# Optimization experiments

Measured on AMD Instinct MI355X. Metric: run time of the kernel, lower is better.

The kernel has to match this reference:

```python
import jax, jax.numpy as jnp
import numpy as np

NUM_HEADS = 12
ROPE_THETA = 10000.0


def _rope_cos_sin(n, hd, dtype):
    inv_freq = 1.0 / (ROPE_THETA ** (np.arange(0, hd, 2, dtype=np.float64) / hd))
    freqs = np.outer(np.arange(n, dtype=np.float64), inv_freq)  # (N, hd/2)
    emb = np.concatenate([freqs, freqs], axis=-1)               # (N, hd)
    return jnp.asarray(np.cos(emb), dtype), jnp.asarray(np.sin(emb), dtype)


def _apply_rope(t, cos, sin):
    # t: (B, H, N, hd); rotate-half convention
    half = t.shape[-1] // 2
    t1, t2 = t[..., :half], t[..., half:]
    rot = jnp.concatenate([-t2, t1], axis=-1)
    return t * cos + rot * sin


def setup_inputs() -> dict:
    key = jax.random.key(0)
    k1, k2, k3 = jax.random.split(key, 3)
    B, N, C = 8, 1024, 768
    x = jax.random.normal(k1, (B, N, C), dtype=jnp.float32)
    w_qkv = jax.random.normal(k2, (C, 3 * C), dtype=jnp.float32) * 0.02
    w_proj = jax.random.normal(k3, (C, C), dtype=jnp.float32) * 0.02
    b_proj = jnp.zeros((C,), dtype=jnp.float32)
    return {"x": x, "w_qkv": w_qkv, "w_proj": w_proj, "b_proj": b_proj}


def reference(x, w_qkv, w_proj, b_proj):
    B, N, C = x.shape
    H = NUM_HEADS
    hd = C // H
    scale = hd ** -0.5
    # qkv: (B,N,3C) -> (B,N,3,H,hd) -> (B,H,3,N,hd)
    qkv = (x @ w_qkv).reshape(B, N, 3, H, hd).transpose(0, 3, 2, 1, 4)
    q, k, v = qkv[:, :, 0], qkv[:, :, 1], qkv[:, :, 2]  # each (B,H,N,hd)
    cos, sin = _rope_cos_sin(N, hd, x.dtype)
    q = _apply_rope(q, cos, sin)
    k = _apply_rope(k, cos, sin)
    attn = jax.nn.softmax(jnp.einsum("bhqd,bhkd->bhqk", q, k) * scale, axis=-1)
    out = jnp.einsum("bhqk,bhkd->bhqd", attn, v)  # (B,H,N,hd)
    out = out.transpose(0, 2, 1, 3).reshape(B, N, C)
    return out @ w_proj + b_proj
```

## Files before the change

### kernel.cpp

```cpp
#include <hip/hip_runtime.h>

typedef unsigned short ushort_t;
typedef __bf16 bf16x8 __attribute__((ext_vector_type(8)));
typedef float f32x4 __attribute__((ext_vector_type(4)));
typedef float f32x16 __attribute__((ext_vector_type(16)));
typedef unsigned short u16x8 __attribute__((ext_vector_type(8)));
typedef unsigned int u32x2 __attribute__((ext_vector_type(2)));
typedef unsigned int u32x4 __attribute__((ext_vector_type(4)));

#define MFMA16(a, b, c) __builtin_amdgcn_mfma_f32_16x16x32_bf16((a), (b), (c), 0, 0, 0)
#define MFMA32(a, b, c) __builtin_amdgcn_mfma_f32_32x32x16_bf16((a), (b), (c), 0, 0, 0)

#define SEQ 1024
#define NHEAD 12
#define HD 64
#define CDIM 768
#define TS 6291456
#define QSCALE 0.1803368801111204f

__device__ __forceinline__ ushort_t f2bf(float f) {
  __bf16 b = (__bf16)f;
  return __builtin_bit_cast(ushort_t, b);
}
__device__ __forceinline__ unsigned pk2(float lo, float hi) {
  return (unsigned)f2bf(lo) | ((unsigned)f2bf(hi) << 16);
}

__device__ __forceinline__ void plswap(unsigned &a, unsigned &b) {
  u32x2 r = __builtin_amdgcn_permlane32_swap(a, b, false, false);
  a = r[0];
  b = r[1];
}

typedef __attribute__((address_space(1))) void gvoid_t;
typedef __attribute__((address_space(3))) void lvoid_t;
__device__ __forceinline__ void async16(const ushort_t* g, ushort_t* l) {
  __builtin_amdgcn_global_load_lds((gvoid_t*)g, (lvoid_t*)l, 16, 0, 0);
}

__device__ __forceinline__ void transpose_body(const float* __restrict__ in,
                                               ushort_t* __restrict__ out,
                                               int R, int C, int bxi, int byi,
                                               float (*tile)[33]) {
  int bx = bxi * 32, by = byi * 32;
  int tx = threadIdx.x & 31, ty = threadIdx.x >> 5;
#pragma unroll
  for (int i = ty; i < 32; i += 8) {
    int r = by + i, c = bx + tx;
    if (r < R && c < C) tile[i][tx] = in[(size_t)r * C + c];
  }
  __syncthreads();
#pragma unroll
  for (int i = ty; i < 32; i += 8) {
    int r = bx + i, c = by + tx;
    if (r < C && c < R) out[(size_t)r * R + c] = f2bf(tile[tx][i]);
  }
}

__global__ void __launch_bounds__(256) prep_all(const float* __restrict__ x,
                                                const float* __restrict__ w_qkv,
                                                const float* __restrict__ w_proj,
                                                ushort_t* __restrict__ xb,
                                                ushort_t* __restrict__ wqkvT,
                                                ushort_t* __restrict__ wprojT,
                                                float* __restrict__ tab) {
  __shared__ float tile[32][33];
  const int bid = blockIdx.x;
  if (bid < 3072) {
    int i = (bid * 256 + threadIdx.x) * 8;
    float4 a = *(const float4*)(x + i);
    float4 b = *(const float4*)(x + i + 4);
    u16x8 r;
    r[0] = f2bf(a.x); r[1] = f2bf(a.y); r[2] = f2bf(a.z); r[3] = f2bf(a.w);
    r[4] = f2bf(b.x); r[5] = f2bf(b.y); r[6] = f2bf(b.z); r[7] = f2bf(b.w);
    *(u16x8*)(xb + i) = r;
  } else if (bid < 3072 + 1728) {
    int t = bid - 3072;
    transpose_body(w_qkv, wqkvT, 768, 2304, t % 72, t / 72, tile);
  } else if (bid < 3072 + 1728 + 576) {
    int t = bid - (3072 + 1728);
    transpose_body(w_proj, wprojT, 768, 768, t % 24, t / 24, tile);
  } else {
    int g = (bid - 5376) * 256 + threadIdx.x;
    int n = g >> 5, j = g & 31;
    double invf = pow(10000.0, -((double)(2 * j)) / 64.0);
    double fr = (double)n * invf;
    tab[g * 2]     = (float)cos(fr);
    tab[g * 2 + 1] = (float)sin(fr);
  }
}

__device__ __forceinline__ void gemm_compute32(const ushort_t* la, const ushort_t* lb,
                                               int wm, int wn, int fr, int fq,
                                               f32x4 acc[4][4]) {
  bf16x8 aF[4], bF[4];
#pragma unroll
  for (int i = 0; i < 4; ++i) {
    const int R = wm + i * 16 + fr;
    aF[i] = *(const bf16x8*)(la + R * 32 + (((fq + (R >> 1)) & 3) << 3));
  }
#pragma unroll
  for (int j = 0; j < 4; ++j) {
    const int S = wn + j * 16 + fr;
    bF[j] = *(const bf16x8*)(lb + S * 32 + (((fq + (S >> 1)) & 3) << 3));
  }
#pragma unroll
  for (int i = 0; i < 4; ++i)
#pragma unroll
    for (int j = 0; j < 4; ++j) acc[i][j] = MFMA16(aF[i], bF[j], acc[i][j]);
}

__device__ __forceinline__ void gemm_bt_core(const ushort_t* __restrict__ A,
                                             const ushort_t* __restrict__ Bt,
                                             int bm, int bn,
                                             ushort_t (*ldsA)[4096],
                                             ushort_t (*ldsB)[4096],
                                             f32x4 acc[4][4]) {
  const int tid = threadIdx.x;
  const int lane = tid & 63, wid = tid >> 6;
  const int wm = (wid >> 1) * 64, wn = (wid & 1) * 64;
  const int fr = lane & 15, fq = lane >> 4;
#pragma unroll
  for (int i = 0; i < 4; ++i)
#pragma unroll
    for (int j = 0; j < 4; ++j) acc[i][j] = (f32x4){0.f, 0.f, 0.f, 0.f};

  const int srow = tid >> 2;
  const int scol = (((tid & 3) - (srow >> 1)) & 3) << 3;
  const ushort_t* aSrc = A + (size_t)(bm + srow) * CDIM + scol;
  const ushort_t* bSrc = Bt + (size_t)(bn + srow) * CDIM + scol;

#define STAGE_STEP(buf, s)                                                       \
  {                                                                              \
    async16(aSrc + (s) * 32, ldsA[buf] + tid * 8);                               \
    async16(aSrc + (size_t)64 * CDIM + (s) * 32, ldsA[buf] + 2048 + tid * 8);    \
    async16(bSrc + (s) * 32, ldsB[buf] + tid * 8);                               \
    async16(bSrc + (size_t)64 * CDIM + (s) * 32, ldsB[buf] + 2048 + tid * 8);    \
  }

  STAGE_STEP(0, 0);
  STAGE_STEP(1, 1);
  STAGE_STEP(2, 2);

#pragma unroll 3
  for (int s = 0; s < 21; ++s) {
    const int b = s % 3;
    asm volatile("s_waitcnt vmcnt(8)" ::: "memory");
    __builtin_amdgcn_sched_barrier(0);
    __builtin_amdgcn_s_barrier();
    __builtin_amdgcn_sched_barrier(0);
    gemm_compute32(ldsA[b], ldsB[b], wm, wn, fr, fq, acc);
    __builtin_amdgcn_sched_barrier(0);
    __builtin_amdgcn_s_barrier();
    __builtin_amdgcn_sched_barrier(0);
    STAGE_STEP(b, s + 3);
  }
  asm volatile("s_waitcnt vmcnt(8)" ::: "memory");
  __builtin_amdgcn_sched_barrier(0);
  __builtin_amdgcn_s_barrier();
  __builtin_amdgcn_sched_barrier(0);
  gemm_compute32(ldsA[0], ldsB[0], wm, wn, fr, fq, acc);
  asm volatile("s_waitcnt vmcnt(4)" ::: "memory");
  __builtin_amdgcn_sched_barrier(0);
  __builtin_amdgcn_s_barrier();
  __builtin_amdgcn_sched_barrier(0);
  gemm_compute32(ldsA[1], ldsB[1], wm, wn, fr, fq, acc);
  asm volatile("s_waitcnt vmcnt(0)" ::: "memory");
  __builtin_amdgcn_sched_barrier(0);
  __builtin_amdgcn_s_barrier();
  __builtin_amdgcn_sched_barrier(0);
  gemm_compute32(ldsA[2], ldsB[2], wm, wn, fr, fq, acc);
#undef STAGE_STEP
}

__global__ void __launch_bounds__(256) gemm_qkv(const ushort_t* __restrict__ A,
                                                const ushort_t* __restrict__ Bt,
                                                const float* __restrict__ tab,
                                                ushort_t* __restrict__ qkv) {
  __shared__ __attribute__((aligned(16))) ushort_t ldsA[3][4096];
  __shared__ __attribute__((aligned(16))) ushort_t ldsB[3][4096];
  f32x4 acc[4][4];
  const int f = blockIdx.x;
  const int xcd = f & 7, r = f >> 3;
  const int bm = (xcd * 8 + (r & 7)) * 128;
  const int bn = (r >> 3) * 128;
  gemm_bt_core(A, Bt, bm, bn, ldsA, ldsB, acc);
  const int lane = threadIdx.x & 63, wid = threadIdx.x >> 6;
  const int wm = (wid >> 1) * 64, wn = (wid & 1) * 64;
  const int fr = lane & 15, fq = lane >> 4;
  const int tensor = bn / 768;

  if (tensor < 2) {
    ushort_t* dstT = qkv + (size_t)tensor * TS;
    const float qs = (tensor == 0) ? QSCALE : 1.0f;
#pragma unroll
    for (int i = 0; i < 4; ++i) {
#pragma unroll
      for (int jp = 0; jp < 2; ++jp) {
        const int col = bn + wn + jp * 16 + fr;
        const int rem = col - tensor * 768;
        const int h = rem >> 6;
        const int d2 = rem & 31;
#pragma unroll
        for (int rr = 0; rr < 4; ++rr) {
          const int row = bm + wm + i * 16 + fq * 4 + rr;
          const int b = row >> 10, n = row & 1023;
          const float2 cs = ((const float2*)tab)[n * 32 + d2];
          const float av = acc[i][jp][rr], bv = acc[i][jp + 2][rr];
          const float o1 = (av * cs.x - bv * cs.y) * qs;
          const float o2 = (bv * cs.x + av * cs.y) * qs;
          ushort_t* dst = dstT + ((size_t)(b * NHEAD + h) * SEQ + n) * HD + d2;
          dst[0]  = f2bf(o1);
          dst[32] = f2bf(o2);
        }
      }
    }
  } else {
    ushort_t* vt = qkv + 2 * (size_t)TS;
#pragma unroll
    for (int i = 0; i < 4; ++i) {
      const int row0 = bm + wm + i * 16 + fq * 4;
      const int b = row0 >> 10, n0 = row0 & 1023;
#pragma unroll
      for (int j = 0; j < 4; ++j) {
        const int col = bn + wn + j * 16 + fr;
        const int rem = col - 1536;
        const int h = rem >> 6, d = rem & 63;
        u32x2 pk;
        pk[0] = pk2(acc[i][j][0], acc[i][j][1]);
        pk[1] = pk2(acc[i][j][2], acc[i][j][3]);
        *(u32x2*)(vt + ((size_t)(b * NHEAD + h) * HD + d) * SEQ + n0) = pk;
      }
    }
  }
}

__global__ void __launch_bounds__(256) gemm_proj(const ushort_t* __restrict__ A,
                                                 const ushort_t* __restrict__ Bt,
                                                 const float* __restrict__ bias,
                                                 float* __restrict__ Cout) {
  __shared__ __attribute__((aligned(16))) ushort_t ldsA[3][4096];
  __shared__ __attribute__((aligned(16))) ushort_t ldsB[3][4096];
  f32x4 acc[4][4];
  const int f = blockIdx.x;
  const int xcd = f & 7, r = f >> 3;
  const int bm = (xcd * 8 + (r & 7)) * 128;
  const int bn = (r >> 3) * 128;
  gemm_bt_core(A, Bt, bm, bn, ldsA, ldsB, acc);
  const int lane = threadIdx.x & 63, wid = threadIdx.x >> 6;
  const int wm = (wid >> 1) * 64, wn = (wid & 1) * 64;
  const int fr = lane & 15, fq = lane >> 4;
#pragma unroll
  for (int i = 0; i < 4; ++i) {
#pragma unroll
    for (int j = 0; j < 4; ++j) {
      const int col = bn + wn + j * 16 + fr;
      const float bv = bias[col];
#pragma unroll
      for (int rr = 0; rr < 4; ++rr) {
        const int row = bm + wm + i * 16 + fq * 4 + rr;
        Cout[(size_t)row * CDIM + col] = acc[i][j][rr] + bv;
      }
    }
  }
}

__global__ void __launch_bounds__(256) attn_fused(const ushort_t* __restrict__ Qb,
                                                  const ushort_t* __restrict__ Kb,
                                                  const ushort_t* __restrict__ VTb,
                                                  ushort_t* __restrict__ Ob) {
  __shared__ __attribute__((aligned(16))) ushort_t ldsK[2][4096];
  __shared__ __attribute__((aligned(16))) ushort_t ldsV[2][4096];

  const int tid = threadIdx.x, lane = tid & 63, wid = tid >> 6;
  const int l31 = lane & 31, h = lane >> 5;

  const int f = blockIdx.x;
  const int xp = f & 7, rest = f >> 3;
  const int g = rest % 12, qb = rest / 12;
  const int head = g * 8 + xp;
  const int q0 = qb * 128;

  const ushort_t* Qh  = Qb  + (size_t)head * (SEQ * HD);
  const ushort_t* Kh  = Kb  + (size_t)head * (SEQ * HD);
  const ushort_t* VTh = VTb + (size_t)head * (HD * SEQ);

  const int qrow = q0 + wid * 32 + l31;
  bf16x8 qF[4];
#pragma unroll
  for (int dk = 0; dk < 4; ++dk)
    qF[dk] = *(const bf16x8*)(Qh + (size_t)qrow * HD + dk * 16 + 8 * h);

  f32x16 ot[2];
#pragma unroll
  for (int dt = 0; dt < 2; ++dt)
#pragma unroll
    for (int i = 0; i < 16; ++i) ot[dt][i] = 0.f;
  float lsum = 0.f;

  const int s0 = tid, s1 = tid + 256;
  const int r0 = s0 >> 3, c0 = ((s0 & 7) - r0) & 7;
  const int r1 = s1 >> 3, c1 = ((s1 & 7) - r1) & 7;

#define ASTAGE(buf, kt)                                                         \
  {                                                                             \
    async16(Kh + (size_t)((kt) * 64 + r0) * HD + c0 * 8, &ldsK[buf][s0 * 8]);   \
    async16(Kh + (size_t)((kt) * 64 + r1) * HD + c1 * 8, &ldsK[buf][s1 * 8]);   \
    async16(VTh + (size_t)r0 * SEQ + (kt) * 64 + c0 * 8, &ldsV[buf][s0 * 8]);   \
    async16(VTh + (size_t)r1 * SEQ + (kt) * 64 + c1 * 8, &ldsV[buf][s1 * 8]);   \
  }

  ASTAGE(0, 0);
  __syncthreads();

  for (int kt = 0; kt < 16; ++kt) {
    const int cur = kt & 1;
    if (kt < 15) ASTAGE(cur ^ 1, kt + 1);

    f32x16 st[2];
    __builtin_amdgcn_s_setprio(1);
#pragma unroll
    for (int ks = 0; ks < 2; ++ks) {
      f32x16 s;
#pragma unroll
      for (int i = 0; i < 16; ++i) s[i] = 0.f;
      const int kr = ks * 32 + l31;
#pragma unroll
      for (int dk = 0; dk < 4; ++dk) {
        const int sw = (dk * 2 + h + kr) & 7;
        bf16x8 kf = *(const bf16x8*)&ldsK[cur][(kr * 8 + sw) * 8];
        s = MFMA32(kf, qF[dk], s);
      }
      st[ks] = s;
    }
    __builtin_amdgcn_s_setprio(0);

    unsigned pk[2][8];
#pragma unroll
    for (int ks = 0; ks < 2; ++ks) {
      float ls = 0.f;
#pragma unroll
      for (int m = 0; m < 8; ++m) {
        const float e0 = __builtin_amdgcn_exp2f(st[ks][2 * m]);
        const float e1 = __builtin_amdgcn_exp2f(st[ks][2 * m + 1]);
        ls += e0 + e1;
        pk[ks][m] = pk2(e0, e1);
      }
      lsum += ls;
    }

#pragma unroll
    for (int kc = 0; kc < 4; ++kc) {
      const int ks = kc >> 1, mb = (kc & 1) * 4;
      unsigned w0 = pk[ks][mb + 0], w2 = pk[ks][mb + 2];
      unsigned w1 = pk[ks][mb + 1], w3 = pk[ks][mb + 3];
      plswap(w0, w2);
      plswap(w1, w3);
      u32x4 bi;
      bi[0] = w0; bi[1] = w1; bi[2] = w2; bi[3] = w3;
      const bf16x8 pf = __builtin_bit_cast(bf16x8, bi);
      __builtin_amdgcn_s_setprio(1);
#pragma unroll
      for (int dt = 0; dt < 2; ++dt) {
        const int dr = dt * 32 + l31;
        const int sw = (kc * 2 + h + dr) & 7;
        bf16x8 vf = *(const bf16x8*)&ldsV[cur][(dr * 8 + sw) * 8];
        ot[dt] = MFMA32(vf, pf, ot[dt]);
      }
      __builtin_amdgcn_s_setprio(0);
    }
    __syncthreads();
  }
#undef ASTAGE

  lsum += __shfl_xor(lsum, 32);
  const float inv = 1.0f / lsum;
  const int b = head / NHEAD, hh = head - b * NHEAD;
  ushort_t* obase = Ob + ((size_t)(b * SEQ + qrow)) * CDIM + hh * HD;
#pragma unroll
  for (int dt = 0; dt < 2; ++dt) {
#pragma unroll
    for (int r2 = 0; r2 < 4; ++r2) {
      const int d = dt * 32 + 8 * r2 + 4 * h;
      u32x2 w;
      w[0] = pk2(ot[dt][4 * r2 + 0] * inv, ot[dt][4 * r2 + 1] * inv);
      w[1] = pk2(ot[dt][4 * r2 + 2] * inv, ot[dt][4 * r2 + 3] * inv);
      *(u32x2*)(obase + d) = w;
    }
  }
}

extern "C" void kernel_launch(void* const* d_in, const int* in_sizes, int n_in,
                              void* d_out, int out_size, void* d_ws, size_t ws_size,
                              hipStream_t stream) {
  const float* x      = (const float*)d_in[0];
  const float* w_qkv  = (const float*)d_in[1];
  const float* w_proj = (const float*)d_in[2];
  const float* b_proj = (const float*)d_in[3];
  float* out = (float*)d_out;
  char* ws = (char*)d_ws;

  ushort_t* xb     = (ushort_t*)(ws + 0);
  ushort_t* wqkvT  = (ushort_t*)(ws + 12582912);
  ushort_t* wprojT = (ushort_t*)(ws + 16121856);
  ushort_t* qkv    = (ushort_t*)(ws + 17301504);
  float*    tab    = (float*)  (ws + 55050240);
  ushort_t* oattn  = (ushort_t*)(ws + 55312384);

  prep_all<<<5504, 256, 0, stream>>>(x, w_qkv, w_proj, xb, wqkvT, wprojT, tab);
  gemm_qkv<<<1152, 256, 0, stream>>>(xb, wqkvT, tab, qkv);
  attn_fused<<<768, 256, 0, stream>>>(qkv, qkv + TS, qkv + 2 * (size_t)TS, oattn);
  gemm_proj<<<384, 256, 0, stream>>>(oattn, wprojT, b_proj, out);
}
```

Before: 196.4 us.

## Rewrite QKV GEMM with 256x256 tiles, 8 waves, double-buffered K-halves

Replaces the 128x128 three-stage gemm_qkv with a 256x256 tile kernel using 512 threads (8 waves, each owning 128x64), a double-buffered LDS pipeline split into two K-halves with interleaved async loads, swizzled LDS chunks, and s_setprio around MFMA bursts. The goal is to raise arithmetic intensity and data reuse per block and to overlap global-to-LDS copies with MFMA work. In exchange it uses 128KB of LDS per block and 288 blocks, which on 256 CUs leaves a partial second wave and low occupancy. The launch_bounds(512,2) hint cannot be met with that much LDS.

```diff
diff --git a/kernel.cpp b/kernel.cpp
--- a/kernel.cpp
+++ b/kernel.cpp
@@ -173,28 +173,135 @@
 #undef STAGE_STEP
 }
 
-__global__ void __launch_bounds__(256) gemm_qkv(const ushort_t* __restrict__ A,
-                                                const ushort_t* __restrict__ Bt,
-                                                const float* __restrict__ tab,
-                                                ushort_t* __restrict__ qkv) {
-  __shared__ __attribute__((aligned(16))) ushort_t ldsA[3][4096];
-  __shared__ __attribute__((aligned(16))) ushort_t ldsB[3][4096];
-  f32x4 acc[4][4];
+__global__ void __launch_bounds__(512, 2) gemm_qkv(const ushort_t* __restrict__ A,
+                                                   const ushort_t* __restrict__ Bt,
+                                                   const float* __restrict__ tab,
+                                                   ushort_t* __restrict__ qkv) {
+  __shared__ __attribute__((aligned(16))) ushort_t lds[65536];
+  const int tid = threadIdx.x, lane = tid & 63;
+  const int wid = tid >> 6, wr = wid >> 2, wc = wid & 3;
+  const int fr = lane & 15, fq = lane >> 4;
+
   const int f = blockIdx.x;
-  const int xcd = f & 7, r = f >> 3;
-  const int bm = (xcd * 8 + (r & 7)) * 128;
-  const int bn = (r >> 3) * 128;
-  gemm_bt_core(A, Bt, bm, bn, ldsA, ldsB, acc);
-  const int lane = threadIdx.x & 63, wid = threadIdx.x >> 6;
-  const int wm = (wid >> 1) * 64, wn = (wid & 1) * 64;
-  const int fr = lane & 15, fq = lane >> 4;
+  const int id = (f & 7) * 36 + (f >> 3);
+  const int mt = id & 31, nt = id >> 5;
+  const int bm = mt * 256, bn = nt * 256;
+
+  const int row0 = tid >> 2, c2 = tid & 3;
+  const int gc = c2 ^ ((row0 >> 1) & 3);
+  const ushort_t* aS = A  + (size_t)(bm + row0) * CDIM + gc * 8;
+  const ushort_t* bS = Bt + (size_t)(bn + row0) * CDIM + gc * 8;
+
+#define AB(buf, kk) (lds + ((buf) * 2 + (kk)) * 8192)
+#define BB(buf, kk) (lds + 32768 + ((buf) * 2 + (kk)) * 8192)
+#define STG_A(nb, kk, tt)                                                     \
+  {                                                                           \
+    async16(aS + (tt) * 64 + (kk) * 32, AB(nb, kk) + tid * 8);                \
+    async16(aS + (size_t)128 * CDIM + (tt) * 64 + (kk) * 32,                  \
+            AB(nb, kk) + 4096 + tid * 8);                                     \
+  }
+#define STG_B(nb, kk, tt)                                                     \
+  {                                                                           \
+    async16(bS + (tt) * 64 + (kk) * 32, BB(nb, kk) + tid * 8);                \
+    async16(bS + (size_t)128 * CDIM + (tt) * 64 + (kk) * 32,                  \
+            BB(nb, kk) + 4096 + tid * 8);                                     \
+  }
+#define WAITBAR(N)                                                            \
+  {                                                                           \
+    asm volatile("s_waitcnt vmcnt(" #N ")" ::: "memory");                     \
+    __builtin_amdgcn_sched_barrier(0);                                        \
+    __builtin_amdgcn_s_barrier();                                             \
+    __builtin_amdgcn_sched_barrier(0);                                        \
+  }
+
+  f32x4 acc[8][4];
+#pragma unroll
+  for (int i = 0; i < 8; ++i)
+#pragma unroll
+    for (int j = 0; j < 4; ++j) acc[i][j] = (f32x4){0.f, 0.f, 0.f, 0.f};
+
+  const int ch = (fq ^ ((fr >> 1) & 3)) << 3;
+  const int ar = wr * 128 + fr;
+  const int br = wc * 64 + fr;
+
+  STG_A(0, 0, 0); STG_B(0, 0, 0); STG_A(0, 1, 0); STG_B(0, 1, 0);
+  WAITBAR(4);
+
+  for (int t = 0; t < 12; ++t) {
+    const int buf = t & 1, nb = buf ^ 1;
+    const bool pre = (t < 11);
+    const ushort_t* lA0 = AB(buf, 0);
+    const ushort_t* lB0 = BB(buf, 0);
+    const ushort_t* lA1 = AB(buf, 1);
+    const ushort_t* lB1 = BB(buf, 1);
+    bf16x8 a[8], b0, b1, b2, b3;
+
+    if (pre) STG_A(nb, 0, t + 1);
+#pragma unroll
+    for (int m = 0; m < 8; ++m)
+      a[m] = *(const bf16x8*)(lA0 + (ar + m * 16) * 32 + ch);
+    b0 = *(const bf16x8*)(lB0 + (br + 0) * 32 + ch);
+    b1 = *(const bf16x8*)(lB0 + (br + 16) * 32 + ch);
+    __builtin_amdgcn_s_setprio(1);
+#pragma unroll
+    for (int m = 0; m < 8; ++m) {
+      acc[m][0] = MFMA16(a[m], b0, acc[m][0]);
+      acc[m][1] = MFMA16(a[m], b1, acc[m][1]);
+    }
+    __builtin_amdgcn_s_setprio(0);
+
+    if (pre) STG_B(nb, 0, t + 1);
+    b2 = *(const bf16x8*)(lB0 + (br + 32) * 32 + ch);
+    b3 = *(const bf16x8*)(lB0 + (br + 48) * 32 + ch);
+    __builtin_amdgcn_s_setprio(1);
+#pragma unroll
+    for (int m = 0; m < 8; ++m) {
+      acc[m][2] = MFMA16(a[m], b2, acc[m][2]);
+      acc[m][3] = MFMA16(a[m], b3, acc[m][3]);
+    }
+    __builtin_amdgcn_s_setprio(0);
+    if (pre) { WAITBAR(4); } else { WAITBAR(0); }
+
+    if (pre) STG_A(nb, 1, t + 1);
+#pragma unroll
+    for (int m = 0; m < 8; ++m)
+      a[m] = *(const bf16x8*)(lA1 + (ar + m * 16) * 32 + ch);
+    b0 = *(const bf16x8*)(lB1 + (br + 0) * 32 + ch);
+    b1 = *(const bf16x8*)(lB1 + (br + 16) * 32 + ch);
+    __builtin_amdgcn_s_setprio(1);
+#pragma unroll
+    for (int m = 0; m < 8; ++m) {
+      acc[m][0] = MFMA16(a[m], b0, acc[m][0]);
+      acc[m][1] = MFMA16(a[m], b1, acc[m][1]);
+    }
+    __builtin_amdgcn_s_setprio(0);
+
+    if (pre) STG_B(nb, 1, t + 1);
+    b2 = *(const bf16x8*)(lB1 + (br + 32) * 32 + ch);
+    b3 = *(const bf16x8*)(lB1 + (br + 48) * 32 + ch);
+    __builtin_amdgcn_s_setprio(1);
+#pragma unroll
+    for (int m = 0; m < 8; ++m) {
+      acc[m][2] = MFMA16(a[m], b2, acc[m][2]);
+      acc[m][3] = MFMA16(a[m], b3, acc[m][3]);
+    }
+    __builtin_amdgcn_s_setprio(0);
+    if (pre) WAITBAR(4);
+  }
+#undef AB
+#undef BB
+#undef STG_A
+#undef STG_B
+#undef WAITBAR
+
+  const int wm = wr * 128, wn = wc * 64;
   const int tensor = bn / 768;
 
   if (tensor < 2) {
     ushort_t* dstT = qkv + (size_t)tensor * TS;
     const float qs = (tensor == 0) ? QSCALE : 1.0f;
 #pragma unroll
-    for (int i = 0; i < 4; ++i) {
+    for (int i = 0; i < 8; ++i) {
 #pragma unroll
       for (int jp = 0; jp < 2; ++jp) {
         const int col = bn + wn + jp * 16 + fr;
@@ -218,9 +325,9 @@
   } else {
     ushort_t* vt = qkv + 2 * (size_t)TS;
 #pragma unroll
-    for (int i = 0; i < 4; ++i) {
-      const int row0 = bm + wm + i * 16 + fq * 4;
-      const int b = row0 >> 10, n0 = row0 & 1023;
+    for (int i = 0; i < 8; ++i) {
+      const int row0v = bm + wm + i * 16 + fq * 4;
+      const int b = row0v >> 10, n0 = row0v & 1023;
 #pragma unroll
       for (int j = 0; j < 4; ++j) {
         const int col = bn + wn + j * 16 + fr;
@@ -408,7 +515,7 @@
   ushort_t* oattn  = (ushort_t*)(ws + 55312384);
 
   prep_all<<<5504, 256, 0, stream>>>(x, w_qkv, w_proj, xb, wqkvT, wprojT, tab);
-  gemm_qkv<<<1152, 256, 0, stream>>>(xb, wqkvT, tab, qkv);
+  gemm_qkv<<<288, 512, 0, stream>>>(xb, wqkvT, tab, qkv);
   attn_fused<<<768, 256, 0, stream>>>(qkv, qkv + TS, qkv + 2 * (size_t)TS, oattn);
   gemm_proj<<<384, 256, 0, stream>>>(oattn, wprojT, b_proj, out);
 }
```

Result: no change. 197.1 us (+0.3%).
